# Kernel optimization log

Measured on AMD Instinct MI355X. Metric: run time of the kernel, lower is better.

The kernel has to match this reference:

```python
import jax, jax.numpy as jnp
import numpy as np

SIZE = (4096, 4096)   # self.size
SIGMA = 1.0           # blur_sigma
NOISE_STD = 0.01      # noise_std


def _gauss_kernel(sigma):
    # scipy.ndimage.gaussian_filter: radius = int(truncate*sigma + 0.5), truncate=4.0
    r = int(4.0 * sigma + 0.5)
    x = np.arange(-r, r + 1, dtype=np.float32)
    k = np.exp(-0.5 * (x / sigma) ** 2)
    k = k / k.sum()
    return jnp.asarray(k), r


def _blur(img, sigma):
    # img: [C, H, W]; separable Gaussian, scipy mode='reflect' == jnp symmetric pad
    k, r = _gauss_kernel(sigma)
    x = jnp.pad(img, ((0, 0), (r, r), (r, r)), mode='symmetric')
    x = x[:, None]  # [C, 1, H+2r, W+2r] (NCHW)
    kh = k.reshape(1, 1, -1, 1)
    kw = k.reshape(1, 1, 1, -1)
    x = jax.lax.conv_general_dilated(x, kh, (1, 1), 'VALID')
    x = jax.lax.conv_general_dilated(x, kw, (1, 1), 'VALID')
    return x[:, 0]  # [C, H, W]


def setup_inputs() -> dict:
    key = jax.random.key(0)
    k1, k2 = jax.random.split(key)
    img = jax.random.normal(k1, (1, 2048, 2048), dtype=jnp.float32)
    noise = jax.random.normal(k2, (1,) + SIZE, dtype=jnp.float32)
    return {"img": img, "noise": noise}


def reference(img, noise):
    # bilinear resize, align_corners=False == jax half-pixel linear resize
    img = jax.image.resize(img, (img.shape[0],) + SIZE, method='linear')
    img = jnp.flip(img, axis=2)   # horizontal flip
    img = jnp.flip(img, axis=1)   # vertical flip
    img = jnp.rot90(img, k=1, axes=(1, 2))  # rot90, k fixed to 1
    img = img + noise * NOISE_STD
    img = _blur(img, SIGMA)
    img = jnp.log1p(jnp.clip(img, 0.0))  # clamp(min=0) then log1p
    return img
```

## Files before the change

### kernel.cpp

```cpp
#include <hip/hip_runtime.h>
#include <math.h>

#define N     4096
#define NIMG  2048
#define TX    56
#define TY    32
#define DW    64
#define DH    40
#define IPP   25
#define STP   41
#define VP    65
#define S2P   59
#define GBX   74
#define GBY   128

#define KW0 0.00013383063f
#define KW1 0.00443186160f
#define KW2 0.05399112800f
#define KW3 0.24197144000f
#define KW4 0.39894346870f

__device__ __forceinline__ int symi(int g) {
    g = (g < 0) ? (-1 - g) : g;
    g = (g >= N) ? (2 * N - 1 - g) : g;
    return g;
}

__global__ __launch_bounds__(256, 4)
void TensorAugment_79216376807666_kernel(const float* __restrict__ img,
                                         const float* __restrict__ noise,
                                         float* __restrict__ out) {
    __shared__ float ST[DW * STP];
    __shared__ float UN[TY * VP];
    float* const IP = UN;
    float* const V  = UN;

    const int tid  = threadIdx.x;
    const int lane = tid & 63;
    const int wave = tid >> 6;

    int b   = blockIdx.y * GBX + blockIdx.x;
    int xcd = b & 7;
    int i   = b >> 3;
    int bx  = i % GBX;
    int by  = xcd * 16 + i / GBX;

    const int x0 = bx * TX;
    const int y0 = by * TY;
    const bool interior = (bx >= 1) && (bx <= 72) && (by >= 1) && (by <= 126);

    const float kk[9] = {KW0, KW1, KW2, KW3, KW4, KW3, KW2, KW1, KW0};

    const int g  = lane & 15;
    const int rr = lane >> 4;
    const int rowbase = wave * 4 + rr;
    float4 nv0, nv1, nv2;
    if (interior) {
        const float* npz = noise + (size_t)(y0 - 4) * N + (x0 - 4) + 4 * g;
        nv0 = *reinterpret_cast<const float4*>(npz + (size_t)rowbase * N);
        nv1 = *reinterpret_cast<const float4*>(npz + (size_t)(rowbase + 16) * N);
        if (rowbase + 32 < DH)
            nv2 = *reinterpret_cast<const float4*>(npz + (size_t)(rowbase + 32) * N);
    }

    int gxa = x0 - 4, gxb = x0 + DW - 5;
    int mxa = symi(gxa), mxb = symi(gxb);
    int gxmin = min(mxa, mxb), gxmax = max(mxa, mxb);
    if (gxa <= 0) gxmin = 0;
    if (gxb >= N - 1) gxmax = N - 1;
    int umin = (N - 1) - gxmax, umax = (N - 1) - gxmin;
    int r0min = (umin - 1) >> 1;
    int r0max = (umax - 1) >> 1;
    int nrows = r0max - r0min + 2;

    int gya = y0 - 4, gyb = y0 + DH - 5;
    int mya = symi(gya), myb = symi(gyb);
    int gymin = min(mya, myb), gymax = max(mya, myb);
    if (gya <= 0) gymin = 0;
    if (gyb >= N - 1) gymax = N - 1;
    int c0min = (gymin - 1) >> 1;
    int c0max = (gymax - 1) >> 1;
    int ncols = c0max - c0min + 2;

    {
        int c = tid & 31;
        for (int r = tid >> 5; r < nrows; r += 8) {
            if (c < ncols) {
                int ir = min(max(r0min + r, 0), NIMG - 1);
                int ic = min(max(c0min + c, 0), NIMG - 1);
                IP[r * IPP + c] = img[ir * NIMG + ic];
            }
        }
    }
    __syncthreads();

    if (interior) {
        int sbase = (30 - 2 * g) * IPP;
        float4 nvv[3] = {nv0, nv1, nv2};
#pragma unroll
        for (int it = 0; it < 3; ++it) {
            int row = it * 16 + rowbase;
            if (row < DH) {
                int jc  = (row + 1) >> 1;
                float wc1 = (row & 1) ? 0.25f : 0.75f;
                float wc0 = 1.0f - wc1;
                float4 nv = nvv[it];
                int bofs = sbase + jc;
                float t0 = fmaf(wc0, IP[bofs],           wc1 * IP[bofs + 1]);
                float t1 = fmaf(wc0, IP[bofs + IPP],     wc1 * IP[bofs + IPP + 1]);
                float t2 = fmaf(wc0, IP[bofs + 2 * IPP], wc1 * IP[bofs + 2 * IPP + 1]);
                float t3 = fmaf(wc0, IP[bofs + 3 * IPP], wc1 * IP[bofs + 3 * IPP + 1]);
                float D0 = fmaf(0.75f, t2, 0.25f * t3);
                float D1 = fmaf(0.25f, t1, 0.75f * t2);
                float D2 = fmaf(0.75f, t1, 0.25f * t2);
                float D3 = fmaf(0.25f, t0, 0.75f * t1);
                int sb = (4 * g) * STP + row;
                ST[sb]           = fmaf(0.01f, nv.x, D0);
                ST[sb + STP]     = fmaf(0.01f, nv.y, D1);
                ST[sb + 2 * STP] = fmaf(0.01f, nv.z, D2);
                ST[sb + 3 * STP] = fmaf(0.01f, nv.w, D3);
            }
        }
    } else {
        int c   = lane;
        int gxm = symi(x0 - 4 + c);
        int u   = (N - 1) - gxm;
        int r0  = (u - 1) >> 1;
        float wr1 = (u & 1) ? 0.25f : 0.75f;
        float wr0 = 1.0f - wr1;
        int a0 = (r0 - r0min) * IPP;
#pragma unroll
        for (int k = 0; k < 10; ++k) {
            int row = wave + 4 * k;
            int gym = symi(y0 - 4 + row);
            int c0  = (gym - 1) >> 1;
            float wc1 = (gym & 1) ? 0.25f : 0.75f;
            float wc0 = 1.0f - wc1;
            int jc = c0 - c0min;
            float nvs = noise[(size_t)gym * N + gxm];
            float f0 = IP[a0 + jc],       f1 = IP[a0 + jc + 1];
            float f2 = IP[a0 + IPP + jc], f3 = IP[a0 + IPP + jc + 1];
            float top = fmaf(wc0, f0, wc1 * f1);
            float bot = fmaf(wc0, f2, wc1 * f3);
            ST[c * STP + row] = fmaf(wr0, top, wr1 * bot) + 0.01f * nvs;
        }
    }
    __syncthreads();

    {
        int c  = lane;
        int rb = wave * 8;
        float win[16];
        int ab = c * STP + rb;
#pragma unroll
        for (int k = 0; k < 16; ++k) win[k] = ST[ab + k];
#pragma unroll
        for (int j = 0; j < 8; ++j) {
            float acc = 0.0f;
#pragma unroll
            for (int i2 = 0; i2 < 9; ++i2) acc = fmaf(kk[i2], win[j + i2], acc);
            V[(rb + j) * VP + c] = acc;
        }
    }
    __syncthreads();

    {
        int r = tid >> 3;
        int s = tid & 7;
        float w2[15];
        int vb = r * VP + s * 7;
#pragma unroll
        for (int k = 0; k < 15; ++k) w2[k] = V[vb + k];
#pragma unroll
        for (int j = 0; j < 7; ++j) {
            float acc = 0.0f;
#pragma unroll
            for (int i2 = 0; i2 < 9; ++i2) acc = fmaf(kk[i2], w2[j + i2], acc);
            acc = fmaxf(acc, 0.0f);
            ST[r * S2P + s * 7 + j] = __logf(1.0f + acc);
        }
    }
    __syncthreads();

    for (int r = wave; r < TY; r += 4) {
        int gx = x0 + lane;
        if (lane < TX && gx < N)
            out[(size_t)(y0 + r) * N + gx] = ST[r * S2P + lane];
    }
}

extern "C" void kernel_launch(void* const* d_in, const int* in_sizes, int n_in,
                              void* d_out, int out_size, void* d_ws, size_t ws_size,
                              hipStream_t stream) {
    const float* img   = (const float*)d_in[0];
    const float* noise = (const float*)d_in[1];
    float* out = (float*)d_out;

    dim3 grid(GBX, GBY);
    TensorAugment_79216376807666_kernel<<<grid, 256, 0, stream>>>(img, noise, out);
}
```

Baseline: 144.0 us.

## Restructure blur into per-wave vertical strips with register-streamed rolling window

Each wavefront now owns a 56x40 output strip and works through it in 8-row chunks. A 16-row register window carries the vertical blur, and the horizontal pass goes through a small per-wave LDS buffer. This removes block-wide __syncthreads and the full-tile staging array, and outputs are written straight to global memory. In exchange it drops the vectorized float4 noise path for interior tiles, which now load noise as scalars, and it changes the grid mapping and occupancy hint.

```diff
diff --git a/kernel.cpp b/kernel.cpp
--- a/kernel.cpp
+++ b/kernel.cpp
@@ -1,18 +1,18 @@
 #include <hip/hip_runtime.h>
 #include <math.h>
 
-#define N     4096
-#define NIMG  2048
-#define TX    56
-#define TY    32
-#define DW    64
-#define DH    40
-#define IPP   25
-#define STP   41
-#define VP    65
-#define S2P   59
-#define GBX   74
-#define GBY   128
+#define N      4096
+#define NIMG   2048
+#define TXO    56
+#define HR     40
+#define DRS    48
+#define IPP    27
+#define IPR    34
+#define VB     64
+#define NSX    74
+#define NSY    103
+#define NSTRIP (NSX * NSY)
+#define NBLK   ((NSTRIP + 3) / 4)
 
 #define KW0 0.00013383063f
 #define KW1 0.00443186160f
@@ -26,44 +26,29 @@
     return g;
 }
 
-__global__ __launch_bounds__(256, 4)
+__global__ __launch_bounds__(256, 5)
 void TensorAugment_79216376807666_kernel(const float* __restrict__ img,
                                          const float* __restrict__ noise,
                                          float* __restrict__ out) {
-    __shared__ float ST[DW * STP];
-    __shared__ float UN[TY * VP];
-    float* const IP = UN;
-    float* const V  = UN;
+    __shared__ float SH[4 * (IPR * IPP + 8 * VB)];
 
     const int tid  = threadIdx.x;
     const int lane = tid & 63;
     const int wave = tid >> 6;
 
-    int b   = blockIdx.y * GBX + blockIdx.x;
-    int xcd = b & 7;
-    int i   = b >> 3;
-    int bx  = i % GBX;
-    int by  = xcd * 16 + i / GBX;
+    float* const IP   = SH + wave * (IPR * IPP + 8 * VB);
+    float* const VBUF = IP + IPR * IPP;
 
-    const int x0 = bx * TX;
-    const int y0 = by * TY;
-    const bool interior = (bx >= 1) && (bx <= 72) && (by >= 1) && (by <= 126);
+    const int strip0 = blockIdx.x * 4 + wave;
+    if (strip0 >= NSTRIP) return;
 
-    const float kk[9] = {KW0, KW1, KW2, KW3, KW4, KW3, KW2, KW1, KW0};
+    const int strip = __builtin_amdgcn_readfirstlane(strip0);
+    const int sx = strip % NSX;
+    const int sy = strip / NSX;
+    const int x0 = sx * TXO;
+    const int y0 = sy * HR;
 
-    const int g  = lane & 15;
-    const int rr = lane >> 4;
-    const int rowbase = wave * 4 + rr;
-    float4 nv0, nv1, nv2;
-    if (interior) {
-        const float* npz = noise + (size_t)(y0 - 4) * N + (x0 - 4) + 4 * g;
-        nv0 = *reinterpret_cast<const float4*>(npz + (size_t)rowbase * N);
-        nv1 = *reinterpret_cast<const float4*>(npz + (size_t)(rowbase + 16) * N);
-        if (rowbase + 32 < DH)
-            nv2 = *reinterpret_cast<const float4*>(npz + (size_t)(rowbase + 32) * N);
-    }
-
-    int gxa = x0 - 4, gxb = x0 + DW - 5;
+    int gxa = x0 - 4, gxb = x0 + 59;
     int mxa = symi(gxa), mxb = symi(gxb);
     int gxmin = min(mxa, mxb), gxmax = max(mxa, mxb);
     if (gxa <= 0) gxmin = 0;
@@ -73,7 +58,7 @@
     int r0max = (umax - 1) >> 1;
     int nrows = r0max - r0min + 2;
 
-    int gya = y0 - 4, gyb = y0 + DH - 5;
+    int gya = y0 - 4, gyb = y0 + DRS - 5;
     int mya = symi(gya), myb = symi(gyb);
     int gymin = min(mya, myb), gymax = max(mya, myb);
     if (gya <= 0) gymin = 0;
@@ -83,109 +68,92 @@
     int ncols = c0max - c0min + 2;
 
     {
-        int c = tid & 31;
-        for (int r = tid >> 5; r < nrows; r += 8) {
-            if (c < ncols) {
-                int ir = min(max(r0min + r, 0), NIMG - 1);
-                int ic = min(max(c0min + c, 0), NIMG - 1);
+        const int c  = lane & 31;
+        const int rb = lane >> 5;
+        const bool cok = (c < ncols);
+#pragma unroll
+        for (int k = 0; k < 17; ++k) {
+            const int r = rb + 2 * k;
+            if (cok && r < nrows) {
+                const int ir = min(max(r0min + r, 0), NIMG - 1);
+                const int ic = min(max(c0min + c, 0), NIMG - 1);
                 IP[r * IPP + c] = img[ir * NIMG + ic];
             }
         }
     }
-    __syncthreads();
 
-    if (interior) {
-        int sbase = (30 - 2 * g) * IPP;
-        float4 nvv[3] = {nv0, nv1, nv2};
+    const int gx  = x0 - 4 + lane;
+    const int gxm = symi(gx);
+    const int u   = (N - 1) - gxm;
+    const int r0  = (u - 1) >> 1;
+    const float wr1 = (u & 1) ? 0.25f : 0.75f;
+    const float wr0 = 1.0f - wr1;
+    const int a0  = (r0 - r0min) * IPP;
+    const bool oklane = (lane >= 4) && (lane < 60) && (gx < N);
+    const int rbase = min(max(lane - 4, 0), VB - 9);
+
+    const float kk[9] = {KW0, KW1, KW2, KW3, KW4, KW3, KW2, KW1, KW0};
+
+    auto nzld = [&](int dr) -> float {
+        const int gym = symi(y0 - 4 + dr);
+        return noise[(size_t)gym * N + gxm];
+    };
+    auto drow = [&](int dr, float nz) -> float {
+        const int gym = symi(y0 - 4 + dr);
+        const int jc  = ((gym - 1) >> 1) - c0min;
+        const float wc1 = (gym & 1) ? 0.25f : 0.75f;
+        const float wc0 = 1.0f - wc1;
+        const float f0 = IP[a0 + jc],       f1 = IP[a0 + jc + 1];
+        const float f2 = IP[a0 + IPP + jc], f3 = IP[a0 + IPP + jc + 1];
+        const float top = fmaf(wc0, f0, wc1 * f1);
+        const float bot = fmaf(wc0, f2, wc1 * f3);
+        return fmaf(0.01f, nz, fmaf(wr0, top, wr1 * bot));
+    };
+
+    float win[16];
+    {
+        float nz[16];
 #pragma unroll
-        for (int it = 0; it < 3; ++it) {
-            int row = it * 16 + rowbase;
-            if (row < DH) {
-                int jc  = (row + 1) >> 1;
-                float wc1 = (row & 1) ? 0.25f : 0.75f;
-                float wc0 = 1.0f - wc1;
-                float4 nv = nvv[it];
-                int bofs = sbase + jc;
-                float t0 = fmaf(wc0, IP[bofs],           wc1 * IP[bofs + 1]);
-                float t1 = fmaf(wc0, IP[bofs + IPP],     wc1 * IP[bofs + IPP + 1]);
-                float t2 = fmaf(wc0, IP[bofs + 2 * IPP], wc1 * IP[bofs + 2 * IPP + 1]);
-                float t3 = fmaf(wc0, IP[bofs + 3 * IPP], wc1 * IP[bofs + 3 * IPP + 1]);
-                float D0 = fmaf(0.75f, t2, 0.25f * t3);
-                float D1 = fmaf(0.25f, t1, 0.75f * t2);
-                float D2 = fmaf(0.75f, t1, 0.25f * t2);
-                float D3 = fmaf(0.25f, t0, 0.75f * t1);
-                int sb = (4 * g) * STP + row;
-                ST[sb]           = fmaf(0.01f, nv.x, D0);
-                ST[sb + STP]     = fmaf(0.01f, nv.y, D1);
-                ST[sb + 2 * STP] = fmaf(0.01f, nv.z, D2);
-                ST[sb + 3 * STP] = fmaf(0.01f, nv.w, D3);
-            }
+        for (int j = 0; j < 16; ++j) nz[j] = nzld(j);
+#pragma unroll
+        for (int j = 0; j < 16; ++j) win[j] = drow(j, nz[j]);
+    }
+
+#pragma unroll 1
+    for (int ck = 2; ck <= 6; ++ck) {
+        float nz[8];
+        if (ck < 6) {
+#pragma unroll
+            for (int j = 0; j < 8; ++j) nz[j] = nzld(8 * ck + j);
         }
-    } else {
-        int c   = lane;
-        int gxm = symi(x0 - 4 + c);
-        int u   = (N - 1) - gxm;
-        int r0  = (u - 1) >> 1;
-        float wr1 = (u & 1) ? 0.25f : 0.75f;
-        float wr0 = 1.0f - wr1;
-        int a0 = (r0 - r0min) * IPP;
-#pragma unroll
-        for (int k = 0; k < 10; ++k) {
-            int row = wave + 4 * k;
-            int gym = symi(y0 - 4 + row);
-            int c0  = (gym - 1) >> 1;
-            float wc1 = (gym & 1) ? 0.25f : 0.75f;
-            float wc0 = 1.0f - wc1;
-            int jc = c0 - c0min;
-            float nvs = noise[(size_t)gym * N + gxm];
-            float f0 = IP[a0 + jc],       f1 = IP[a0 + jc + 1];
-            float f2 = IP[a0 + IPP + jc], f3 = IP[a0 + IPP + jc + 1];
-            float top = fmaf(wc0, f0, wc1 * f1);
-            float bot = fmaf(wc0, f2, wc1 * f3);
-            ST[c * STP + row] = fmaf(wr0, top, wr1 * bot) + 0.01f * nvs;
-        }
-    }
-    __syncthreads();
 
-    {
-        int c  = lane;
-        int rb = wave * 8;
-        float win[16];
-        int ab = c * STP + rb;
-#pragma unroll
-        for (int k = 0; k < 16; ++k) win[k] = ST[ab + k];
 #pragma unroll
         for (int j = 0; j < 8; ++j) {
-            float acc = 0.0f;
+            float acc = kk[0] * win[j];
 #pragma unroll
-            for (int i2 = 0; i2 < 9; ++i2) acc = fmaf(kk[i2], win[j + i2], acc);
-            V[(rb + j) * VP + c] = acc;
+            for (int i = 1; i < 9; ++i) acc = fmaf(kk[i], win[j + i], acc);
+            VBUF[j * VB + lane] = acc;
         }
-    }
-    __syncthreads();
 
-    {
-        int r = tid >> 3;
-        int s = tid & 7;
-        float w2[15];
-        int vb = r * VP + s * 7;
+        const int gyb0 = y0 + 8 * (ck - 2);
 #pragma unroll
-        for (int k = 0; k < 15; ++k) w2[k] = V[vb + k];
+        for (int j = 0; j < 8; ++j) {
+            const int vb = j * VB + rbase;
+            float acc = kk[0] * VBUF[vb];
 #pragma unroll
-        for (int j = 0; j < 7; ++j) {
-            float acc = 0.0f;
+            for (int i = 1; i < 9; ++i) acc = fmaf(kk[i], VBUF[vb + i], acc);
+            acc = fmaxf(acc, 0.0f);
+            const float r = __logf(1.0f + acc);
+            const int gy = gyb0 + j;
+            if (oklane && gy < N) out[(size_t)gy * N + gx] = r;
+        }
+
+        if (ck < 6) {
 #pragma unroll
-            for (int i2 = 0; i2 < 9; ++i2) acc = fmaf(kk[i2], w2[j + i2], acc);
-            acc = fmaxf(acc, 0.0f);
-            ST[r * S2P + s * 7 + j] = __logf(1.0f + acc);
+            for (int i = 0; i < 8; ++i) win[i] = win[i + 8];
+#pragma unroll
+            for (int j = 0; j < 8; ++j) win[8 + j] = drow(8 * ck + j, nz[j]);
         }
-    }
-    __syncthreads();
-
-    for (int r = wave; r < TY; r += 4) {
-        int gx = x0 + lane;
-        if (lane < TX && gx < N)
-            out[(size_t)(y0 + r) * N + gx] = ST[r * S2P + lane];
     }
 }
 
@@ -196,6 +164,6 @@
     const float* noise = (const float*)d_in[1];
     float* out = (float*)d_out;
 
-    dim3 grid(GBX, GBY);
+    dim3 grid(NBLK);
     TensorAugment_79216376807666_kernel<<<grid, 256, 0, stream>>>(img, noise, out);
 }
```

After: 149.0 us. 1.03x slower.
